# Kernel optimization log

Measured on AMD Instinct MI355X. Metric: run time of the kernel, lower is better.

## Reference

```python
import jax, jax.numpy as jnp
import numpy as np
import math

S, B, D, H = 2048, 2, 1024, 16
DK = D // H


def setup_inputs() -> dict:
    key = jax.random.key(0)
    ks = jax.random.split(key, 13)
    scale = 1.0 / math.sqrt(D)
    inp = {
        "query": jax.random.normal(ks[0], (S, B, D), jnp.float32),
        "key": jax.random.normal(ks[1], (S, B, D), jnp.float32),
        "value": jax.random.normal(ks[2], (S, B, D), jnp.float32),
        "mask": jax.random.normal(ks[3], (B, S, S), jnp.float32),
        # four Linear(d_model, d_model) layers: q, k, v, out. torch convention W:(out,in)
        "Wq": jax.random.normal(ks[4], (D, D), jnp.float32) * scale,
        "bq": jax.random.normal(ks[5], (D,), jnp.float32) * scale,
        "Wk": jax.random.normal(ks[6], (D, D), jnp.float32) * scale,
        "bk": jax.random.normal(ks[7], (D,), jnp.float32) * scale,
        "Wv": jax.random.normal(ks[8], (D, D), jnp.float32) * scale,
        "bv": jax.random.normal(ks[9], (D,), jnp.float32) * scale,
        "Wo": jax.random.normal(ks[10], (D, D), jnp.float32) * scale,
        "bo": jax.random.normal(ks[11], (D,), jnp.float32) * scale,
    }
    return inp


def reference(query, key, value, mask, Wq, bq, Wk, bk, Wv, bv, Wo, bo):
    # inputs are (tokens S, batch B, d_model D)
    def proj(x, W, b):  # torch Linear: x @ W.T + b, then split heads -> (B,H,S,DK)
        y = jnp.einsum('sbd,ed->sbe', x, W) + b
        return y.reshape(S, B, H, DK).transpose(1, 2, 0, 3)

    q = proj(query, Wq, bq)
    k = proj(key, Wk, bk)
    v = proj(value, Wv, bv)

    scores = jnp.einsum('bhsd,bhtd->bhst', q, k) / math.sqrt(DK)
    scores = scores + mask[:, None, :, :]  # broadcast over heads
    p_attn = jax.nn.softmax(scores, axis=-1)  # (B,H,S,S)

    x = jnp.einsum('bhst,bhtd->bhsd', p_attn, v)  # (B,H,S,DK)
    x = x.transpose(2, 0, 1, 3).reshape(S, B, D)  # (S,B,D)
    out = jnp.einsum('sbd,ed->sbe', x, Wo) + bo

    attn = p_attn.mean(axis=1)  # mean over heads -> (B,S,S)
    return out, attn
```

## Files before the change

### kernel.cpp

```cpp
#include <hip/hip_runtime.h>
#include <hip/hip_bf16.h>


#define S_LEN 2048
#define BATCH 2
#define DMODEL 1024
#define NH 16
#define DKH 64
#define SCALE 0.125f
#define FMAX 20.0f
#define KSTRIDE 72

typedef __bf16 bf16_t;
typedef __attribute__((ext_vector_type(8))) __bf16 bf16x8;
typedef __attribute__((ext_vector_type(8))) unsigned short u16x8;
typedef __attribute__((ext_vector_type(4))) float f32x4;

__device__ __forceinline__ unsigned short f32_bf16_rne(float f) {
  union { float f; unsigned int u; } v; v.f = f;
  unsigned int u = v.u;
  u += 0x7fffu + ((u >> 16) & 1u);
  return (unsigned short)(u >> 16);
}
__device__ __forceinline__ float bf16u_f32(unsigned short us) {
  union { unsigned int u; float f; } v; v.u = ((unsigned int)us) << 16;
  return v.f;
}
__device__ __forceinline__ f32x4 mfma_bf16(bf16x8 a, bf16x8 b, f32x4 c) {
  return __builtin_amdgcn_mfma_f32_16x16x32_bf16(a, b, c, 0, 0, 0);
}
__device__ __forceinline__ void gload16(const bf16_t* g, unsigned short* l) {
  __builtin_amdgcn_global_load_lds(
      (const __attribute__((address_space(1))) void*)g,
      (__attribute__((address_space(3))) void*)l, 16, 0, 0);
}

__global__ __launch_bounds__(256) void cvt_w_kernel(
    const float* __restrict__ w0, const float* __restrict__ w1,
    const float* __restrict__ w2, const float* __restrict__ w3,
    bf16_t* __restrict__ o0, bf16_t* __restrict__ o1,
    bf16_t* __restrict__ o2, bf16_t* __restrict__ o3) {
  const float* src; bf16_t* dst;
  switch (blockIdx.y) {
    case 0: src = w0; dst = o0; break;
    case 1: src = w1; dst = o1; break;
    case 2: src = w2; dst = o2; break;
    default: src = w3; dst = o3; break;
  }
  int i = (blockIdx.x * 256 + threadIdx.x) * 4;
  float4 v = *(const float4*)(src + i);
  union { unsigned short u[4]; uint2 q; } r;
  r.u[0] = f32_bf16_rne(v.x); r.u[1] = f32_bf16_rne(v.y);
  r.u[2] = f32_bf16_rne(v.z); r.u[3] = f32_bf16_rne(v.w);
  *(uint2*)(dst + i) = r.q;
}

__global__ __launch_bounds__(256) void cvt_x_kernel(
    const float* __restrict__ x0, const float* __restrict__ x1,
    const float* __restrict__ x2,
    bf16_t* __restrict__ o0, bf16_t* __restrict__ o1, bf16_t* __restrict__ o2) {
  const float* src; bf16_t* dst;
  switch (blockIdx.y) {
    case 0: src = x0; dst = o0; break;
    case 1: src = x1; dst = o1; break;
    default: src = x2; dst = o2; break;
  }
  int i = (blockIdx.x * 256 + threadIdx.x) * 4;
  float4 v = *(const float4*)(src + i);
  union { unsigned short u[4]; uint2 q; } r;
  r.u[0] = f32_bf16_rne(v.x); r.u[1] = f32_bf16_rne(v.y);
  r.u[2] = f32_bf16_rne(v.z); r.u[3] = f32_bf16_rne(v.w);
  *(uint2*)(dst + i) = r.q;
}

__global__ __launch_bounds__(256) void cvt_mask_kernel(
    const float* __restrict__ m, bf16_t* __restrict__ o) {
  int i = (blockIdx.x * 256 + threadIdx.x) * 4;
  float4 v = *(const float4*)(m + i);
  union { unsigned short u[4]; uint2 q; } r;
  r.u[0] = f32_bf16_rne(v.x); r.u[1] = f32_bf16_rne(v.y);
  r.u[2] = f32_bf16_rne(v.z); r.u[3] = f32_bf16_rne(v.w);
  *(uint2*)(o + i) = r.q;
}

__global__ __launch_bounds__(256) void proj_kernel(
    const bf16_t* __restrict__ Xq, const bf16_t* __restrict__ Xk, const bf16_t* __restrict__ Xv,
    const bf16_t* __restrict__ Wqb, const bf16_t* __restrict__ Wkb, const bf16_t* __restrict__ Wvb,
    const float* __restrict__ bq, const float* __restrict__ bk, const float* __restrict__ bv,
    bf16_t* __restrict__ qo, bf16_t* __restrict__ ko, bf16_t* __restrict__ vTo) {
  int mode = blockIdx.z;
  const bf16_t* X = (mode == 0) ? Xq : (mode == 1) ? Xk : Xv;
  const bf16_t* W = (mode == 0) ? Wqb : (mode == 1) ? Wkb : Wvb;
  const float* bias = (mode == 0) ? bq : (mode == 1) ? bk : bv;

  __shared__ __align__(16) unsigned short Alds[128 * 32];
  __shared__ __align__(16) unsigned short Blds[128 * 32];

  int tid = threadIdx.x;
  int wv = tid >> 6, lane = tid & 63, quad = lane >> 4, col = lane & 15;
  int wr = wv >> 1, wc = wv & 1;
  int rowbase = blockIdx.x * 128;
  int colbase = blockIdx.y * 128;

  int srow = tid >> 2;
  int sk8 = (tid & 3) * 8;
  const bf16_t* ga0 = X + (size_t)(rowbase + srow) * DMODEL + sk8;
  const bf16_t* gb0 = W + (size_t)(colbase + srow) * DMODEL + sk8;
  unsigned short* la0 = Alds + tid * 8;
  unsigned short* lb0 = Blds + tid * 8;

  f32x4 acc[4][4] = {};

  for (int k0 = 0; k0 < DMODEL; k0 += 32) {
    gload16(ga0 + k0, la0);
    gload16(ga0 + 64 * DMODEL + k0, la0 + 2048);
    gload16(gb0 + k0, lb0);
    gload16(gb0 + 64 * DMODEL + k0, lb0 + 2048);
    __syncthreads();

    union { u16x8 u; bf16x8 v; } af[4], bfr[4];
#pragma unroll
    for (int mi = 0; mi < 4; ++mi)
      af[mi].u = *(const u16x8*)(Alds + (wr * 64 + mi * 16 + col) * 32 + quad * 8);
#pragma unroll
    for (int ni = 0; ni < 4; ++ni)
      bfr[ni].u = *(const u16x8*)(Blds + (wc * 64 + ni * 16 + col) * 32 + quad * 8);
#pragma unroll
    for (int mi = 0; mi < 4; ++mi)
#pragma unroll
      for (int ni = 0; ni < 4; ++ni)
        acc[mi][ni] = mfma_bf16(af[mi].v, bfr[ni].v, acc[mi][ni]);
    __syncthreads();
  }

  float biasv[4];
#pragma unroll
  for (int ni = 0; ni < 4; ++ni)
    biasv[ni] = bias[colbase + wc * 64 + ni * 16 + col];

#pragma unroll
  for (int mi = 0; mi < 4; ++mi)
#pragma unroll
    for (int ni = 0; ni < 4; ++ni)
#pragma unroll
      for (int r = 0; r < 4; ++r) {
        int grow = rowbase + wr * 64 + mi * 16 + quad * 4 + r;
        int gcol = colbase + wc * 64 + ni * 16 + col;
        unsigned short us = f32_bf16_rne(acc[mi][ni][r] + biasv[ni]);
        int s = grow >> 1, bb = grow & 1;
        int h = gcol >> 6, dk = gcol & 63;
        if (mode == 2) {
          ((unsigned short*)vTo)[((size_t)(bb * NH + h) * DKH + dk) * S_LEN + s] = us;
        } else {
          unsigned short* dst = (unsigned short*)(mode == 0 ? qo : ko);
          dst[((size_t)(bb * NH + h) * S_LEN + s) * DKH + dk] = us;
        }
      }
}

__global__ __launch_bounds__(512) void flash_kernel(
    const bf16_t* __restrict__ maskb,
    const bf16_t* __restrict__ q_ws, const bf16_t* __restrict__ k_ws,
    const bf16_t* __restrict__ vT_ws,
    bf16_t* __restrict__ x_ws, float* __restrict__ rl_ws) {
  int tid = threadIdx.x;
  int w = tid >> 6, lane = tid & 63, quad = lane >> 4, col = lane & 15;
  int b = blockIdx.y, h = blockIdx.z;
  int s0 = blockIdx.x * 128 + w * 16;
  int bh = b * NH + h;

  __shared__ __align__(16) unsigned short Klds[64 * KSTRIDE];
  __shared__ __align__(16) unsigned short Vlds[64 * KSTRIDE];
  __shared__ __align__(16) unsigned short Plds[8][16 * KSTRIDE];
  unsigned short* pw = &Plds[w][0];

  const bf16_t* qh = q_ws + (size_t)bh * S_LEN * DKH;
  const bf16_t* kh = k_ws + (size_t)bh * S_LEN * DKH;
  const bf16_t* vh = vT_ws + (size_t)bh * DKH * S_LEN;
  const unsigned short* mrow = (const unsigned short*)maskb +
      (size_t)b * S_LEN * S_LEN + (size_t)(s0 + quad * 4) * S_LEN;

  bf16x8 qf0 = *(const bf16x8*)(qh + (s0 + col) * DKH + quad * 8);
  bf16x8 qf1 = *(const bf16x8*)(qh + (s0 + col) * DKH + 32 + quad * 8);

  int srow = w * 8 + (lane >> 3), schunk = lane & 7;
  const u16x8* kg = (const u16x8*)(kh + (size_t)srow * DKH + schunk * 8);
  const u16x8* vg = (const u16x8*)(vh + (size_t)srow * S_LEN + schunk * 8);
  u16x8* kl = (u16x8*)(Klds + srow * KSTRIDE + schunk * 8);
  u16x8* vl = (u16x8*)(Vlds + srow * KSTRIDE + schunk * 8);

  f32x4 xacc[4] = {};
  f32x4 lacc = {};

  for (int t0 = 0; t0 < S_LEN; t0 += 64) {
    *kl = *(const u16x8*)((const unsigned short*)kg + (size_t)t0 * DKH);
    *vl = *(const u16x8*)((const unsigned short*)vg + t0);
    __syncthreads();

    f32x4 C[4];
    for (int j = 0; j < 4; ++j) {
      int row = j * 16 + col;
      union { u16x8 u; bf16x8 v; } kb0, kb1;
      kb0.u = *(const u16x8*)(Klds + row * KSTRIDE + quad * 8);
      kb1.u = *(const u16x8*)(Klds + row * KSTRIDE + 32 + quad * 8);
      f32x4 z = {};
      C[j] = mfma_bf16(qf1, kb1.v, mfma_bf16(qf0, kb0.v, z));
    }

    for (int j = 0; j < 4; ++j)
      for (int r = 0; r < 4; ++r) {
        float mk = bf16u_f32(mrow[r * S_LEN + t0 + j * 16 + col]) - FMAX;
        float p = __expf(C[j][r] * SCALE + mk);
        lacc[r] += p;
        pw[(quad * 4 + r) * KSTRIDE + j * 16 + col] = f32_bf16_rne(p);
      }

    union { u16x8 u; bf16x8 v; } pa0, pa1;
    pa0.u = *(const u16x8*)(pw + col * KSTRIDE + quad * 8);
    pa1.u = *(const u16x8*)(pw + col * KSTRIDE + 32 + quad * 8);

    for (int ni = 0; ni < 4; ++ni) {
      int row = ni * 16 + col;
      union { u16x8 u; bf16x8 v; } vb0, vb1;
      vb0.u = *(const u16x8*)(Vlds + row * KSTRIDE + quad * 8);
      vb1.u = *(const u16x8*)(Vlds + row * KSTRIDE + 32 + quad * 8);
      xacc[ni] = mfma_bf16(pa1.v, vb1.v, mfma_bf16(pa0.v, vb0.v, xacc[ni]));
    }
    __syncthreads();
  }

  for (int d = 1; d < 16; d <<= 1)
    for (int r = 0; r < 4; ++r) lacc[r] += __shfl_xor(lacc[r], d, 64);
  float rl[4];
  for (int r = 0; r < 4; ++r) rl[r] = 1.0f / lacc[r];

  unsigned short* xo = (unsigned short*)x_ws;
  for (int ni = 0; ni < 4; ++ni)
    for (int r = 0; r < 4; ++r) {
      int sr = s0 + quad * 4 + r;
      xo[((size_t)bh * S_LEN + sr) * DKH + ni * 16 + col] =
          f32_bf16_rne(xacc[ni][r] * rl[r]);
    }
  if (col == 0)
    for (int r = 0; r < 4; ++r)
      rl_ws[bh * S_LEN + s0 + quad * 4 + r] = rl[r];
}

__global__ __launch_bounds__(256) void attn_kernel(
    const bf16_t* __restrict__ maskb,
    const bf16_t* __restrict__ q_ws, const bf16_t* __restrict__ k_ws,
    const float* __restrict__ rl_ws,
    float* __restrict__ attn_out) {
  int tid = threadIdx.x;
  int w = tid >> 6, lane = tid & 63, quad = lane >> 4, col = lane & 15;
  int b = blockIdx.y;
  int s0 = blockIdx.x * 64 + w * 16;
  int t_base = blockIdx.z * 128;

  __shared__ __align__(16) unsigned short Klds[128 * KSTRIDE];

  const unsigned short* mrow = (const unsigned short*)maskb +
      (size_t)b * S_LEN * S_LEN + (size_t)(s0 + quad * 4) * S_LEN + t_base;
  float mk[8][4];
  for (int j = 0; j < 8; ++j)
    for (int r = 0; r < 4; ++r)
      mk[j][r] = bf16u_f32(mrow[r * S_LEN + j * 16 + col]) - FMAX;

  f32x4 acc[8] = {};

  for (int h = 0; h < NH; ++h) {
    int bh = b * NH + h;
    const bf16_t* qh = q_ws + (size_t)bh * S_LEN * DKH;
    const bf16_t* kh = k_ws + (size_t)bh * S_LEN * DKH;

    for (int i = 0; i < 4; ++i) {
      int row = i * 32 + w * 8 + (lane >> 3);
      int chunk = lane & 7;
      *(u16x8*)(Klds + row * KSTRIDE + chunk * 8) =
          *(const u16x8*)(kh + (size_t)(t_base + row) * DKH + chunk * 8);
    }
    __syncthreads();

    bf16x8 qf0 = *(const bf16x8*)(qh + (s0 + col) * DKH + quad * 8);
    bf16x8 qf1 = *(const bf16x8*)(qh + (s0 + col) * DKH + 32 + quad * 8);
    float rl4[4];
    for (int r = 0; r < 4; ++r) rl4[r] = rl_ws[bh * S_LEN + s0 + quad * 4 + r];

    for (int j = 0; j < 8; ++j) {
      int row = j * 16 + col;
      union { u16x8 u; bf16x8 v; } kb0, kb1;
      kb0.u = *(const u16x8*)(Klds + row * KSTRIDE + quad * 8);
      kb1.u = *(const u16x8*)(Klds + row * KSTRIDE + 32 + quad * 8);
      f32x4 z = {};
      f32x4 C = mfma_bf16(qf1, kb1.v, mfma_bf16(qf0, kb0.v, z));
      for (int r = 0; r < 4; ++r)
        acc[j][r] += __expf(C[r] * SCALE + mk[j][r]) * rl4[r];
    }
    __syncthreads();
  }

  for (int j = 0; j < 8; ++j)
    for (int r = 0; r < 4; ++r)
      attn_out[((size_t)b * S_LEN + s0 + quad * 4 + r) * S_LEN + t_base + j * 16 + col] =
          acc[j][r] * (1.0f / NH);
}

__global__ __launch_bounds__(256) void outproj_kernel(
    const bf16_t* __restrict__ x_ws, const bf16_t* __restrict__ Wob,
    const float* __restrict__ bo, float* __restrict__ out) {
  __shared__ __align__(16) unsigned short Alds[128 * 32];
  __shared__ __align__(16) unsigned short Blds[128 * 32];

  int tid = threadIdx.x;
  int wv = tid >> 6, lane = tid & 63, quad = lane >> 4, col = lane & 15;
  int wr = wv >> 1, wc = wv & 1;
  int rowbase = blockIdx.x * 128;
  int colbase = blockIdx.y * 128;

  int srow = tid >> 2;
  int sk8 = (tid & 3) * 8;
  int r0 = rowbase + srow;
  int s0a = r0 >> 1, b0a = r0 & 1;
  int r1 = r0 + 64;
  int s1a = r1 >> 1, b1a = r1 & 1;
  const bf16_t* gb0 = Wob + (size_t)(colbase + srow) * DMODEL + sk8;
  unsigned short* la0 = Alds + tid * 8;
  unsigned short* lb0 = Blds + tid * 8;

  f32x4 acc[4][4] = {};

  for (int k0 = 0; k0 < DMODEL; k0 += 32) {
    int h = k0 >> 6, dk = (k0 & 63) + sk8;
    gload16(x_ws + ((size_t)(b0a * NH + h) * S_LEN + s0a) * DKH + dk, la0);
    gload16(x_ws + ((size_t)(b1a * NH + h) * S_LEN + s1a) * DKH + dk, la0 + 2048);
    gload16(gb0 + k0, lb0);
    gload16(gb0 + 64 * DMODEL + k0, lb0 + 2048);
    __syncthreads();

    union { u16x8 u; bf16x8 v; } af[4], bfr[4];
#pragma unroll
    for (int mi = 0; mi < 4; ++mi)
      af[mi].u = *(const u16x8*)(Alds + (wr * 64 + mi * 16 + col) * 32 + quad * 8);
#pragma unroll
    for (int ni = 0; ni < 4; ++ni)
      bfr[ni].u = *(const u16x8*)(Blds + (wc * 64 + ni * 16 + col) * 32 + quad * 8);
#pragma unroll
    for (int mi = 0; mi < 4; ++mi)
#pragma unroll
      for (int ni = 0; ni < 4; ++ni)
        acc[mi][ni] = mfma_bf16(af[mi].v, bfr[ni].v, acc[mi][ni]);
    __syncthreads();
  }

  float biasv[4];
#pragma unroll
  for (int ni = 0; ni < 4; ++ni)
    biasv[ni] = bo[colbase + wc * 64 + ni * 16 + col];

#pragma unroll
  for (int mi = 0; mi < 4; ++mi)
#pragma unroll
    for (int ni = 0; ni < 4; ++ni)
#pragma unroll
      for (int r = 0; r < 4; ++r) {
        int grow = rowbase + wr * 64 + mi * 16 + quad * 4 + r;
        int gcol = colbase + wc * 64 + ni * 16 + col;
        out[(size_t)grow * DMODEL + gcol] = acc[mi][ni][r] + biasv[ni];
      }
}

extern "C" void kernel_launch(void* const* d_in, const int* in_sizes, int n_in,
                              void* d_out, int out_size, void* d_ws, size_t ws_size,
                              hipStream_t stream) {
  const float* query = (const float*)d_in[0];
  const float* key_  = (const float*)d_in[1];
  const float* value = (const float*)d_in[2];
  const float* mask  = (const float*)d_in[3];
  const float* Wq = (const float*)d_in[4];
  const float* bq = (const float*)d_in[5];
  const float* Wk = (const float*)d_in[6];
  const float* bk = (const float*)d_in[7];
  const float* Wv = (const float*)d_in[8];
  const float* bv = (const float*)d_in[9];
  const float* Wo = (const float*)d_in[10];
  const float* bo = (const float*)d_in[11];

  char* ws = (char*)d_ws;
  bf16_t* q_ws  = (bf16_t*)(ws + 0);
  bf16_t* k_ws  = (bf16_t*)(ws + 8388608);
  bf16_t* vT_ws = (bf16_t*)(ws + 16777216);
  bf16_t* x_ws  = (bf16_t*)(ws + 25165824);
  float*  rl_ws = (float*)(ws + 33554432);
  bf16_t* Wqb = (bf16_t*)(ws + 33816576);
  bf16_t* Wkb = (bf16_t*)(ws + 35913728);
  bf16_t* Wvb = (bf16_t*)(ws + 38010880);
  bf16_t* Wob = (bf16_t*)(ws + 40108032);
  bf16_t* Xq_b = x_ws;
  bf16_t* Xk_b = (bf16_t*)(ws + 42205184);
  bf16_t* Xv_b = (bf16_t*)(ws + 50593792);
  bf16_t* maskb = (bf16_t*)(ws + 42205184);

  float* outp  = (float*)d_out;
  float* attnp = outp + (size_t)S_LEN * BATCH * DMODEL;

  cvt_w_kernel<<<dim3(1024, 4), 256, 0, stream>>>(Wq, Wk, Wv, Wo, Wqb, Wkb, Wvb, Wob);
  cvt_x_kernel<<<dim3(4096, 3), 256, 0, stream>>>(query, key_, value, Xq_b, Xk_b, Xv_b);
  proj_kernel<<<dim3(32, 8, 3), 256, 0, stream>>>(Xq_b, Xk_b, Xv_b,
                                                  Wqb, Wkb, Wvb, bq, bk, bv,
                                                  q_ws, k_ws, vT_ws);
  cvt_mask_kernel<<<dim3(8192), 256, 0, stream>>>(mask, maskb);
  flash_kernel<<<dim3(16, 2, 16), 512, 0, stream>>>(maskb, q_ws, k_ws, vT_ws, x_ws, rl_ws);
  attn_kernel<<<dim3(32, 2, 16), 256, 0, stream>>>(maskb, q_ws, k_ws, rl_ws, attnp);
  outproj_kernel<<<dim3(32, 8), 256, 0, stream>>>(x_ws, Wob, bo, outp);
}
```

Measured before the change: 352.5 us.

## Precompute exp(mask), fold softmax scale into Q, prefetch K/V tiles, swizzle P

The mask is now converted once into exp(mask - FMAX) in bf16, and Q is prescaled by SCALE*log2(e), so the flash and attention kernels compute each probability as exp2(score) times the stored mask factor instead of a full exp with a scale and mask add. K/V tiles are software-prefetched into registers one iteration ahead in both kernels. P stores to LDS use an XOR swizzle and packed bf16 conversion to cut bank conflicts, and the inner loops are unrolled. Storing exp(mask) in bf16 changes rounding behaviour and raises register pressure.

```diff
diff --git a/kernel.cpp b/kernel.cpp
--- a/kernel.cpp
+++ b/kernel.cpp
@@ -8,6 +8,7 @@
 #define NH 16
 #define DKH 64
 #define SCALE 0.125f
+#define QSCALE 0.180336878f
 #define FMAX 20.0f
 #define KSTRIDE 72
 
@@ -28,6 +29,13 @@
 }
 __device__ __forceinline__ f32x4 mfma_bf16(bf16x8 a, bf16x8 b, f32x4 c) {
   return __builtin_amdgcn_mfma_f32_16x16x32_bf16(a, b, c, 0, 0, 0);
+}
+__device__ __forceinline__ float exp2_fast(float x) {
+#if __has_builtin(__builtin_amdgcn_exp2f)
+  return __builtin_amdgcn_exp2f(x);
+#else
+  return __expf(x * 0.69314718f);
+#endif
 }
 __device__ __forceinline__ void gload16(const bf16_t* g, unsigned short* l) {
   __builtin_amdgcn_global_load_lds(
@@ -78,8 +86,10 @@
   int i = (blockIdx.x * 256 + threadIdx.x) * 4;
   float4 v = *(const float4*)(m + i);
   union { unsigned short u[4]; uint2 q; } r;
-  r.u[0] = f32_bf16_rne(v.x); r.u[1] = f32_bf16_rne(v.y);
-  r.u[2] = f32_bf16_rne(v.z); r.u[3] = f32_bf16_rne(v.w);
+  r.u[0] = f32_bf16_rne(__expf(v.x - FMAX));
+  r.u[1] = f32_bf16_rne(__expf(v.y - FMAX));
+  r.u[2] = f32_bf16_rne(__expf(v.z - FMAX));
+  r.u[3] = f32_bf16_rne(__expf(v.w - FMAX));
   *(uint2*)(o + i) = r.q;
 }
 
@@ -146,7 +156,9 @@
       for (int r = 0; r < 4; ++r) {
         int grow = rowbase + wr * 64 + mi * 16 + quad * 4 + r;
         int gcol = colbase + wc * 64 + ni * 16 + col;
-        unsigned short us = f32_bf16_rne(acc[mi][ni][r] + biasv[ni]);
+        float val = acc[mi][ni][r] + biasv[ni];
+        if (mode == 0) val *= QSCALE;
+        unsigned short us = f32_bf16_rne(val);
         int s = grow >> 1, bb = grow & 1;
         int h = gcol >> 6, dk = gcol & 63;
         if (mode == 2) {
@@ -159,7 +171,7 @@
 }
 
 __global__ __launch_bounds__(512) void flash_kernel(
-    const bf16_t* __restrict__ maskb,
+    const bf16_t* __restrict__ emb,
     const bf16_t* __restrict__ q_ws, const bf16_t* __restrict__ k_ws,
     const bf16_t* __restrict__ vT_ws,
     bf16_t* __restrict__ x_ws, float* __restrict__ rl_ws) {
@@ -177,27 +189,46 @@
   const bf16_t* qh = q_ws + (size_t)bh * S_LEN * DKH;
   const bf16_t* kh = k_ws + (size_t)bh * S_LEN * DKH;
   const bf16_t* vh = vT_ws + (size_t)bh * DKH * S_LEN;
-  const unsigned short* mrow = (const unsigned short*)maskb +
+  const unsigned short* emrow = (const unsigned short*)emb +
       (size_t)b * S_LEN * S_LEN + (size_t)(s0 + quad * 4) * S_LEN;
 
   bf16x8 qf0 = *(const bf16x8*)(qh + (s0 + col) * DKH + quad * 8);
   bf16x8 qf1 = *(const bf16x8*)(qh + (s0 + col) * DKH + 32 + quad * 8);
 
   int srow = w * 8 + (lane >> 3), schunk = lane & 7;
-  const u16x8* kg = (const u16x8*)(kh + (size_t)srow * DKH + schunk * 8);
-  const u16x8* vg = (const u16x8*)(vh + (size_t)srow * S_LEN + schunk * 8);
+  const unsigned short* kg = (const unsigned short*)(kh + (size_t)srow * DKH + schunk * 8);
+  const unsigned short* vg = (const unsigned short*)(vh + (size_t)srow * S_LEN + schunk * 8);
   u16x8* kl = (u16x8*)(Klds + srow * KSTRIDE + schunk * 8);
   u16x8* vl = (u16x8*)(Vlds + srow * KSTRIDE + schunk * 8);
 
+  int psw = (quad & 2) ? 16 : 0;
+  int rsw = (col & 8) ? 16 : 0;
+
   f32x4 xacc[4] = {};
   f32x4 lacc = {};
 
+  u16x8 kpre = *(const u16x8*)kg;
+  u16x8 vpre = *(const u16x8*)vg;
+
   for (int t0 = 0; t0 < S_LEN; t0 += 64) {
-    *kl = *(const u16x8*)((const unsigned short*)kg + (size_t)t0 * DKH);
-    *vl = *(const u16x8*)((const unsigned short*)vg + t0);
-    __syncthreads();
+    *kl = kpre;
+    *vl = vpre;
+    __syncthreads();
+
+    if (t0 + 64 < S_LEN) {
+      kpre = *(const u16x8*)(kg + (size_t)(t0 + 64) * DKH);
+      vpre = *(const u16x8*)(vg + (t0 + 64));
+    }
+
+    float emv[4][4];
+#pragma unroll
+    for (int j = 0; j < 4; ++j)
+#pragma unroll
+      for (int r = 0; r < 4; ++r)
+        emv[j][r] = bf16u_f32(emrow[r * S_LEN + t0 + j * 16 + col]);
 
     f32x4 C[4];
+#pragma unroll
     for (int j = 0; j < 4; ++j) {
       int row = j * 16 + col;
       union { u16x8 u; bf16x8 v; } kb0, kb1;
@@ -207,18 +238,29 @@
       C[j] = mfma_bf16(qf1, kb1.v, mfma_bf16(qf0, kb0.v, z));
     }
 
-    for (int j = 0; j < 4; ++j)
-      for (int r = 0; r < 4; ++r) {
-        float mk = bf16u_f32(mrow[r * S_LEN + t0 + j * 16 + col]) - FMAX;
-        float p = __expf(C[j][r] * SCALE + mk);
-        lacc[r] += p;
-        pw[(quad * 4 + r) * KSTRIDE + j * 16 + col] = f32_bf16_rne(p);
-      }
+#pragma unroll
+    for (int j = 0; j < 4; ++j) {
+      float p0 = exp2_fast(C[j][0]) * emv[j][0];
+      float p1 = exp2_fast(C[j][1]) * emv[j][1];
+      float p2 = exp2_fast(C[j][2]) * emv[j][2];
+      float p3 = exp2_fast(C[j][3]) * emv[j][3];
+      lacc[0] += p0; lacc[1] += p1; lacc[2] += p2; lacc[3] += p3;
+      unsigned int w01, w23;
+      asm("v_cvt_pk_bf16_f32 %0, %1, %2" : "=v"(w01) : "v"(p0), "v"(p1));
+      asm("v_cvt_pk_bf16_f32 %0, %1, %2" : "=v"(w23) : "v"(p2), "v"(p3));
+      int tsw = (j * 16 + col) ^ psw;
+      int rb = quad * 4;
+      pw[(rb + 0) * KSTRIDE + tsw] = (unsigned short)(w01 & 0xffffu);
+      pw[(rb + 1) * KSTRIDE + tsw] = (unsigned short)(w01 >> 16);
+      pw[(rb + 2) * KSTRIDE + tsw] = (unsigned short)(w23 & 0xffffu);
+      pw[(rb + 3) * KSTRIDE + tsw] = (unsigned short)(w23 >> 16);
+    }
 
     union { u16x8 u; bf16x8 v; } pa0, pa1;
-    pa0.u = *(const u16x8*)(pw + col * KSTRIDE + quad * 8);
-    pa1.u = *(const u16x8*)(pw + col * KSTRIDE + 32 + quad * 8);
-
+    pa0.u = *(const u16x8*)(pw + col * KSTRIDE + ((quad * 8) ^ rsw));
+    pa1.u = *(const u16x8*)(pw + col * KSTRIDE + (32 + ((quad * 8) ^ rsw)));
+
+#pragma unroll
     for (int ni = 0; ni < 4; ++ni) {
       int row = ni * 16 + col;
       union { u16x8 u; bf16x8 v; } vb0, vb1;
@@ -247,7 +289,7 @@
 }
 
 __global__ __launch_bounds__(256) void attn_kernel(
-    const bf16_t* __restrict__ maskb,
+    const bf16_t* __restrict__ emb,
     const bf16_t* __restrict__ q_ws, const bf16_t* __restrict__ k_ws,
     const float* __restrict__ rl_ws,
     float* __restrict__ attn_out) {
@@ -259,33 +301,45 @@
 
   __shared__ __align__(16) unsigned short Klds[128 * KSTRIDE];
 
-  const unsigned short* mrow = (const unsigned short*)maskb +
+  const unsigned short* emrow = (const unsigned short*)emb +
       (size_t)b * S_LEN * S_LEN + (size_t)(s0 + quad * 4) * S_LEN + t_base;
-  float mk[8][4];
+  float emf[8][4];
   for (int j = 0; j < 8; ++j)
     for (int r = 0; r < 4; ++r)
-      mk[j][r] = bf16u_f32(mrow[r * S_LEN + j * 16 + col]) - FMAX;
+      emf[j][r] = bf16u_f32(emrow[r * S_LEN + j * 16 + col]);
 
   f32x4 acc[8] = {};
+
+  int srow_a = w * 8 + (lane >> 3), schunk_a = (lane & 7) * 8;
+  const bf16_t* kh0 = k_ws + (size_t)(b * NH) * S_LEN * DKH;
+
+  u16x8 kpre[4];
+#pragma unroll
+  for (int i = 0; i < 4; ++i)
+    kpre[i] = *(const u16x8*)(kh0 + (size_t)(t_base + i * 32 + srow_a) * DKH + schunk_a);
 
   for (int h = 0; h < NH; ++h) {
     int bh = b * NH + h;
     const bf16_t* qh = q_ws + (size_t)bh * S_LEN * DKH;
-    const bf16_t* kh = k_ws + (size_t)bh * S_LEN * DKH;
-
-    for (int i = 0; i < 4; ++i) {
-      int row = i * 32 + w * 8 + (lane >> 3);
-      int chunk = lane & 7;
-      *(u16x8*)(Klds + row * KSTRIDE + chunk * 8) =
-          *(const u16x8*)(kh + (size_t)(t_base + row) * DKH + chunk * 8);
-    }
-    __syncthreads();
+
+#pragma unroll
+    for (int i = 0; i < 4; ++i)
+      *(u16x8*)(Klds + (i * 32 + srow_a) * KSTRIDE + schunk_a) = kpre[i];
+    __syncthreads();
+
+    if (h + 1 < NH) {
+      const bf16_t* khn = kh0 + (size_t)(h + 1) * S_LEN * DKH;
+#pragma unroll
+      for (int i = 0; i < 4; ++i)
+        kpre[i] = *(const u16x8*)(khn + (size_t)(t_base + i * 32 + srow_a) * DKH + schunk_a);
+    }
 
     bf16x8 qf0 = *(const bf16x8*)(qh + (s0 + col) * DKH + quad * 8);
     bf16x8 qf1 = *(const bf16x8*)(qh + (s0 + col) * DKH + 32 + quad * 8);
     float rl4[4];
     for (int r = 0; r < 4; ++r) rl4[r] = rl_ws[bh * S_LEN + s0 + quad * 4 + r];
 
+#pragma unroll
     for (int j = 0; j < 8; ++j) {
       int row = j * 16 + col;
       union { u16x8 u; bf16x8 v; } kb0, kb1;
@@ -293,8 +347,11 @@
       kb1.u = *(const u16x8*)(Klds + row * KSTRIDE + 32 + quad * 8);
       f32x4 z = {};
       f32x4 C = mfma_bf16(qf1, kb1.v, mfma_bf16(qf0, kb0.v, z));
-      for (int r = 0; r < 4; ++r)
-        acc[j][r] += __expf(C[r] * SCALE + mk[j][r]) * rl4[r];
+#pragma unroll
+      for (int r = 0; r < 4; ++r) {
+        float t = exp2_fast(C[r]) * emf[j][r];
+        acc[j][r] = fmaf(t, rl4[r], acc[j][r]);
+      }
     }
     __syncthreads();
   }
@@ -398,7 +455,7 @@
   bf16_t* Xq_b = x_ws;
   bf16_t* Xk_b = (bf16_t*)(ws + 42205184);
   bf16_t* Xv_b = (bf16_t*)(ws + 50593792);
-  bf16_t* maskb = (bf16_t*)(ws + 42205184);
+  bf16_t* emb  = (bf16_t*)(ws + 42205184);
 
   float* outp  = (float*)d_out;
   float* attnp = outp + (size_t)S_LEN * BATCH * DMODEL;
@@ -408,8 +465,8 @@
   proj_kernel<<<dim3(32, 8, 3), 256, 0, stream>>>(Xq_b, Xk_b, Xv_b,
                                                   Wqb, Wkb, Wvb, bq, bk, bv,
                                                   q_ws, k_ws, vT_ws);
-  cvt_mask_kernel<<<dim3(8192), 256, 0, stream>>>(mask, maskb);
-  flash_kernel<<<dim3(16, 2, 16), 512, 0, stream>>>(maskb, q_ws, k_ws, vT_ws, x_ws, rl_ws);
-  attn_kernel<<<dim3(32, 2, 16), 256, 0, stream>>>(maskb, q_ws, k_ws, rl_ws, attnp);
+  cvt_mask_kernel<<<dim3(8192), 256, 0, stream>>>(mask, emb);
+  flash_kernel<<<dim3(16, 2, 16), 512, 0, stream>>>(emb, q_ws, k_ws, vT_ws, x_ws, rl_ws);
+  attn_kernel<<<dim3(32, 2, 16), 256, 0, stream>>>(emb, q_ws, k_ws, rl_ws, attnp);
   outproj_kernel<<<dim3(32, 8), 256, 0, stream>>>(x_ws, Wob, bo, outp);
 }
```

Result: no change. 350.3 us (-0.6%).
